# Optimization experiments

Measured on AMD Instinct MI355X. Metric: run time of the kernel, lower is better.

## Reference

```python
import jax, jax.numpy as jnp
import numpy as np

PADDING = 1
STRIDE = 1

def setup_inputs() -> dict:
    key = jax.random.key(0)
    k1, k2 = jax.random.split(key)
    x = jax.random.normal(k1, (32, 64, 64, 64), dtype=jnp.float32)
    # kaiming_normal fan_out, relu: std = sqrt(2 / (out_ch * k * k))
    fan_out = 128 * 3 * 3
    std = np.sqrt(2.0 / fan_out).astype(np.float32)
    weight = jax.random.normal(k2, (128, 64, 3, 3), dtype=jnp.float32) * std
    bias = jnp.zeros((128,), dtype=jnp.float32)
    return {"x": x, "weight": weight, "bias": bias}

def reference(x, weight, bias):
    # Faithful to the unfold+multiply+sum path, which computes a standard
    # cross-correlation conv2d (torch conv semantics) with stride/padding.
    out = jax.lax.conv_general_dilated(
        x, weight,
        window_strides=(STRIDE, STRIDE),
        padding=[(PADDING, PADDING), (PADDING, PADDING)],
        dimension_numbers=("NCHW", "OIHW", "NCHW"),
    )
    return out + bias[None, :, None, None]
```

## Files before the change

### kernel.cpp

```cpp
#include <hip/hip_runtime.h>


typedef short short8 __attribute__((ext_vector_type(8)));
typedef float f32x4  __attribute__((ext_vector_type(4)));

static __device__ __forceinline__ unsigned short f2bf(float f) {
    unsigned int u = __float_as_uint(f);
    u = (u + 0x7FFFu + ((u >> 16) & 1u)) >> 16;
    return (unsigned short)u;
}
static __device__ __forceinline__ unsigned int pk2(float lo, float hi) {
    return (unsigned int)f2bf(lo) | ((unsigned int)f2bf(hi) << 16);
}

__global__ __launch_bounds__(256)
void prep_x(const float* __restrict__ x, unsigned short* __restrict__ xT)
{
    __shared__ float T[64][65];
    const int h = blockIdx.x, n = blockIdx.y, tid = threadIdx.x;
    const size_t nbase = (size_t)n * 262144 + (size_t)h * 64;
    #pragma unroll
    for (int i = 0; i < 16; ++i) {
        int idx = tid + i * 256;
        int ci = idx >> 6, w = idx & 63;
        T[ci][w] = x[nbase + (size_t)ci * 4096 + w];
    }
    __syncthreads();
    const int w = tid >> 2, cg = tid & 3;
    unsigned int pk[8];
    #pragma unroll
    for (int k = 0; k < 8; ++k)
        pk[k] = pk2(T[cg * 16 + 2 * k][w], T[cg * 16 + 2 * k + 1][w]);
    unsigned short* dst = xT + (((size_t)n * 64 + h) * 64 + w) * 64 + cg * 16;
    uint4 a; a.x = pk[0]; a.y = pk[1]; a.z = pk[2]; a.w = pk[3];
    uint4 b; b.x = pk[4]; b.y = pk[5]; b.z = pk[6]; b.w = pk[7];
    *(uint4*)(dst)     = a;
    *(uint4*)(dst + 8) = b;
}

__global__ __launch_bounds__(256)
void prep_w(const float* __restrict__ w, unsigned short* __restrict__ wA)
{
    int t = blockIdx.x * 256 + threadIdx.x;
    if (t >= 73728) return;
    int j    = t & 7;
    int lane = (t >> 3) & 63;
    int mf   = (t >> 9) & 3;
    int c    = (t >> 11) & 1;
    int rest = t >> 12;
    int p    = rest % 9;
    int cb   = rest / 9;
    int co = cb * 64 + mf * 16 + (lane & 15);
    int ci = c * 32 + (lane >> 4) * 8 + j;
    wA[t] = f2bf(w[(size_t)(co * 64 + ci) * 9 + p]);
}

__global__ __launch_bounds__(512, 4)
void conv_mfma5(const unsigned short* __restrict__ xT,
                const unsigned short* __restrict__ wA,
                const float* __restrict__ bias,
                float* __restrict__ out)
{
    __shared__ __align__(16) char lds[50688];

    const int tid  = threadIdx.x;
    const int h0   = blockIdx.x * 4;
    const int n    = blockIdx.y;
    const int wid  = tid >> 6;
    const int cb   = wid >> 2;
    const int wrow = wid & 3;
    const int lane = tid & 63;
    const int l15  = lane & 15, l4 = lane >> 4;

    const unsigned short* xTn = xT + (size_t)n * 262144;
    const unsigned short* wAb = wA + (size_t)cb * 36864;

    {
        uint4 xreg[7];
        #pragma unroll
        for (int k = 0; k < 7; ++k) {
            int G = tid + k * 512;
            if (k < 6 || tid < 96) {
                int hp = G / 528, rem = G - hp * 528;
                int wp = rem >> 3, g = rem & 7;
                int gh = h0 + hp - 1, gw = wp - 1;
                uint4 v; v.x = v.y = v.z = v.w = 0u;
                if ((unsigned)gh < 64u && (unsigned)gw < 64u)
                    v = *(const uint4*)(xTn + ((gh * 64 + gw) * 64 + g * 8));
                xreg[k] = v;
            }
        }
        #pragma unroll
        for (int k = 0; k < 7; ++k) {
            int G = tid + k * 512;
            if (k < 6 || tid < 96) {
                int hp = G / 528, rem = G - hp * 528;
                int wp = rem >> 3, g = rem & 7;
                *(uint4*)(lds + (hp * 66 + wp) * 128 + ((g ^ (wp & 7)) * 16)) = xreg[k];
            }
        }
    }
    __syncthreads();

    f32x4 acc[4][4];
    #pragma unroll
    for (int mf = 0; mf < 4; ++mf)
        #pragma unroll
        for (int nf = 0; nf < 4; ++nf)
            acc[mf][nf] = (f32x4)0.0f;

    #pragma unroll
    for (int p = 0; p < 9; ++p) {
        const int kh = p / 3, kw = p - kh * 3;
        #pragma unroll
        for (int c = 0; c < 2; ++c) {
            short8 Af[4], Bf[4];
            #pragma unroll
            for (int mf = 0; mf < 4; ++mf)
                Af[mf] = *(const short8*)(wAb + ((((p * 2 + c) * 4 + mf) * 64 + lane) << 3));
            #pragma unroll
            for (int nf = 0; nf < 4; ++nf) {
                const int hp = wrow + kh;
                const int wp = nf * 16 + l15 + kw;
                Bf[nf] = *(const short8*)(lds + (hp * 66 + wp) * 128 + (((c * 4 + l4) ^ (wp & 7)) * 16));
            }
            __builtin_amdgcn_s_setprio(1);
            #pragma unroll
            for (int mf = 0; mf < 4; ++mf)
                #pragma unroll
                for (int nf = 0; nf < 4; ++nf)
                    acc[mf][nf] = __builtin_amdgcn_mfma_f32_16x16x32_bf16(
                        Af[mf], Bf[nf], acc[mf][nf], 0, 0, 0);
            __builtin_amdgcn_s_setprio(0);
        }
    }

    {
        const int h = h0 + wrow;
        #pragma unroll
        for (int mf = 0; mf < 4; ++mf) {
            const f32x4 bv4 = *(const f32x4*)(bias + cb * 64 + mf * 16 + l4 * 4);
            #pragma unroll
            for (int r = 0; r < 4; ++r) {
                const int co = cb * 64 + mf * 16 + l4 * 4 + r;
                float* orow = out + (((size_t)n * 128 + co) * 64 + h) * 64;
                const float bv = bv4[r];
                #pragma unroll
                for (int nf = 0; nf < 4; ++nf)
                    orow[nf * 16 + l15] = acc[mf][nf][r] + bv;
            }
        }
    }
}

__global__ __launch_bounds__(256, 4)
void conv2d_f32_tiled(const float* __restrict__ x,
                      const float* __restrict__ wgt,
                      const float* __restrict__ bias,
                      float* __restrict__ out)
{
    __shared__ float Xlds[8][10][66];
    __shared__ float Wlds[32][72];
    const int tid = threadIdx.x;
    const int co0 = blockIdx.x * 32, h0 = blockIdx.y * 8, n = blockIdx.z;
    const int tco = tid >> 6, lane = tid & 63;
    float acc[8][8];
    #pragma unroll
    for (int i = 0; i < 8; ++i)
        #pragma unroll
        for (int j = 0; j < 8; ++j) acc[i][j] = 0.0f;
    for (int cc = 0; cc < 8; ++cc) {
        const int ci0 = cc * 8;
        for (int idx = tid; idx < 8 * 10 * 66; idx += 256) {
            const int ww = idx % 66, t = idx / 66, hh = t % 10, ci = t / 10;
            const int gh = h0 + hh - 1, gw = ww - 1;
            float v = 0.0f;
            if ((unsigned)gh < 64u && (unsigned)gw < 64u)
                v = x[(((size_t)n * 64 + ci0 + ci) * 64 + gh) * 64 + gw];
            Xlds[ci][hh][ww] = v;
        }
        for (int idx = tid; idx < 32 * 72; idx += 256) {
            const int r = idx % 72, co = idx / 72;
            Wlds[co][r] = wgt[(size_t)(co0 + co) * 576 + ci0 * 9 + r];
        }
        __syncthreads();
        for (int ci = 0; ci < 8; ++ci)
            #pragma unroll
            for (int kh = 0; kh < 3; ++kh)
                #pragma unroll
                for (int kw = 0; kw < 3; ++kw) {
                    float wv[8];
                    #pragma unroll
                    for (int i = 0; i < 8; ++i) wv[i] = Wlds[tco * 8 + i][ci * 9 + kh * 3 + kw];
                    #pragma unroll
                    for (int j = 0; j < 8; ++j) {
                        const float xv = Xlds[ci][j + kh][lane + kw];
                        #pragma unroll
                        for (int i = 0; i < 8; ++i) acc[i][j] = fmaf(wv[i], xv, acc[i][j]);
                    }
                }
        __syncthreads();
    }
    #pragma unroll
    for (int i = 0; i < 8; ++i) {
        const int co = co0 + tco * 8 + i;
        const float b = bias[co];
        #pragma unroll
        for (int j = 0; j < 8; ++j)
            out[(((size_t)n * 128 + co) * 64 + (h0 + j)) * 64 + lane] = acc[i][j] + b;
    }
}

extern "C" void kernel_launch(void* const* d_in, const int* in_sizes, int n_in,
                              void* d_out, int out_size, void* d_ws, size_t ws_size,
                              hipStream_t stream)
{
    const float* x    = (const float*)d_in[0];
    const float* wgt  = (const float*)d_in[1];
    const float* bias = (const float*)d_in[2];
    float* out        = (float*)d_out;

    const size_t XT_BYTES = (size_t)32 * 64 * 64 * 64 * 2;
    const size_t WT_BYTES = (size_t)128 * 576 * 2;

    if (ws_size < XT_BYTES + WT_BYTES) {
        dim3 grid(4, 8, 32);
        conv2d_f32_tiled<<<grid, 256, 0, stream>>>(x, wgt, bias, out);
        return;
    }

    unsigned short* xT = (unsigned short*)d_ws;
    unsigned short* wA = (unsigned short*)((char*)d_ws + XT_BYTES);

    prep_x<<<dim3(64, 32), 256, 0, stream>>>(x, xT);
    prep_w<<<dim3((73728 + 255) / 256), 256, 0, stream>>>(wgt, wA);
    conv_mfma5<<<dim3(16, 32), 512, 0, stream>>>(xT, wA, bias, out);
}
```

Before: 42.71 us.

## Stage weights in LDS and double output rows per block in MFMA conv

The conv kernel now covers 8 output rows per block instead of 4, which doubles each wave's N tile to 8 fragments and halves the grid to 256 blocks. Weights are stored in a plain co-major bf16 layout. Each kernel-row phase stages them into swizzled LDS, and the next phase's weights are prefetched into registers while the current phase computes. The aim is to replace repeated global weight reads per MFMA step with LDS reads and to amortise the halo overhead. In exchange the kernel uses about 130KB of dynamic LDS and more accumulator registers, which lowers occupancy. There are also extra barriers, and 256 blocks may underfill the 256 CUs.

```diff
diff --git a/kernel.cpp b/kernel.cpp
--- a/kernel.cpp
+++ b/kernel.cpp
@@ -39,32 +39,30 @@
 }
 
 __global__ __launch_bounds__(256)
-void prep_w(const float* __restrict__ w, unsigned short* __restrict__ wA)
+void prep_w(const float* __restrict__ w, unsigned short* __restrict__ wT)
 {
     int t = blockIdx.x * 256 + threadIdx.x;
-    if (t >= 73728) return;
-    int j    = t & 7;
-    int lane = (t >> 3) & 63;
-    int mf   = (t >> 9) & 3;
-    int c    = (t >> 11) & 1;
-    int rest = t >> 12;
-    int p    = rest % 9;
-    int cb   = rest / 9;
-    int co = cb * 64 + mf * 16 + (lane & 15);
-    int ci = c * 32 + (lane >> 4) * 8 + j;
-    wA[t] = f2bf(w[(size_t)(co * 64 + ci) * 9 + p]);
-}
-
-__global__ __launch_bounds__(512, 4)
-void conv_mfma5(const unsigned short* __restrict__ xT,
-                const unsigned short* __restrict__ wA,
+    if (t >= 128 * 576) return;
+    int co = t / 576, r = t - co * 576;
+    int p = r >> 6, ci = r & 63;
+    wT[t] = f2bf(w[(size_t)(co * 64 + ci) * 9 + p]);
+}
+
+#define XBYTES 84480
+#define WBYTES 49152
+#define TOTAL_LDS (XBYTES + WBYTES)
+
+__global__ __launch_bounds__(512, 2)
+void conv_mfma7(const unsigned short* __restrict__ xT,
+                const unsigned short* __restrict__ wT,
                 const float* __restrict__ bias,
                 float* __restrict__ out)
 {
-    __shared__ __align__(16) char lds[50688];
+    extern __shared__ __align__(16) char lds[];
+    char* wl = lds + XBYTES;
 
     const int tid  = threadIdx.x;
-    const int h0   = blockIdx.x * 4;
+    const int h0   = blockIdx.x * 8;
     const int n    = blockIdx.y;
     const int wid  = tid >> 6;
     const int cb   = wid >> 2;
@@ -73,14 +71,29 @@
     const int l15  = lane & 15, l4 = lane >> 4;
 
     const unsigned short* xTn = xT + (size_t)n * 262144;
-    const unsigned short* wAb = wA + (size_t)cb * 36864;
 
     {
-        uint4 xreg[7];
-        #pragma unroll
-        for (int k = 0; k < 7; ++k) {
-            int G = tid + k * 512;
-            if (k < 6 || tid < 96) {
+        uint4 wreg[6];
+        #pragma unroll
+        for (int k = 0; k < 6; ++k) {
+            int G = tid + k * 512;
+            int g = G & 7, co = (G >> 3) & 127, pl = G >> 10;
+            wreg[k] = *(const uint4*)(wT + co * 576 + (pl * 64 + g * 8));
+        }
+        #pragma unroll
+        for (int k = 0; k < 6; ++k) {
+            int G = tid + k * 512;
+            int g = G & 7, co = (G >> 3) & 127, pl = G >> 10;
+            *(uint4*)(wl + (pl * 128 + co) * 128 + ((g ^ (co & 7)) * 16)) = wreg[k];
+        }
+    }
+
+    {
+        uint4 xreg[11];
+        #pragma unroll
+        for (int k = 0; k < 11; ++k) {
+            int G = tid + k * 512;
+            if (k < 10 || tid < 160) {
                 int hp = G / 528, rem = G - hp * 528;
                 int wp = rem >> 3, g = rem & 7;
                 int gh = h0 + hp - 1, gw = wp - 1;
@@ -91,9 +104,9 @@
             }
         }
         #pragma unroll
-        for (int k = 0; k < 7; ++k) {
-            int G = tid + k * 512;
-            if (k < 6 || tid < 96) {
+        for (int k = 0; k < 11; ++k) {
+            int G = tid + k * 512;
+            if (k < 10 || tid < 160) {
                 int hp = G / 528, rem = G - hp * 528;
                 int wp = rem >> 3, g = rem & 7;
                 *(uint4*)(lds + (hp * 66 + wp) * 128 + ((g ^ (wp & 7)) * 16)) = xreg[k];
@@ -102,52 +115,78 @@
     }
     __syncthreads();
 
-    f32x4 acc[4][4];
+    f32x4 acc[4][8];
     #pragma unroll
     for (int mf = 0; mf < 4; ++mf)
         #pragma unroll
-        for (int nf = 0; nf < 4; ++nf)
+        for (int nf = 0; nf < 8; ++nf)
             acc[mf][nf] = (f32x4)0.0f;
 
     #pragma unroll
-    for (int p = 0; p < 9; ++p) {
-        const int kh = p / 3, kw = p - kh * 3;
-        #pragma unroll
-        for (int c = 0; c < 2; ++c) {
-            short8 Af[4], Bf[4];
-            #pragma unroll
-            for (int mf = 0; mf < 4; ++mf)
-                Af[mf] = *(const short8*)(wAb + ((((p * 2 + c) * 4 + mf) * 64 + lane) << 3));
-            #pragma unroll
-            for (int nf = 0; nf < 4; ++nf) {
-                const int hp = wrow + kh;
-                const int wp = nf * 16 + l15 + kw;
-                Bf[nf] = *(const short8*)(lds + (hp * 66 + wp) * 128 + (((c * 4 + l4) ^ (wp & 7)) * 16));
-            }
-            __builtin_amdgcn_s_setprio(1);
-            #pragma unroll
-            for (int mf = 0; mf < 4; ++mf)
-                #pragma unroll
-                for (int nf = 0; nf < 4; ++nf)
-                    acc[mf][nf] = __builtin_amdgcn_mfma_f32_16x16x32_bf16(
-                        Af[mf], Bf[nf], acc[mf][nf], 0, 0, 0);
-            __builtin_amdgcn_s_setprio(0);
-        }
-    }
-
-    {
-        const int h = h0 + wrow;
-        #pragma unroll
-        for (int mf = 0; mf < 4; ++mf) {
-            const f32x4 bv4 = *(const f32x4*)(bias + cb * 64 + mf * 16 + l4 * 4);
-            #pragma unroll
-            for (int r = 0; r < 4; ++r) {
-                const int co = cb * 64 + mf * 16 + l4 * 4 + r;
-                float* orow = out + (((size_t)n * 128 + co) * 64 + h) * 64;
-                const float bv = bv4[r];
-                #pragma unroll
-                for (int nf = 0; nf < 4; ++nf)
-                    orow[nf * 16 + l15] = acc[mf][nf][r] + bv;
+    for (int ph = 0; ph < 3; ++ph) {
+        uint4 wreg[6];
+        if (ph < 2) {
+            #pragma unroll
+            for (int k = 0; k < 6; ++k) {
+                int G = tid + k * 512;
+                int g = G & 7, co = (G >> 3) & 127, pl = G >> 10;
+                wreg[k] = *(const uint4*)(wT + co * 576 + (((ph + 1) * 3 + pl) * 64 + g * 8));
+            }
+        }
+
+        #pragma unroll
+        for (int pl = 0; pl < 3; ++pl) {
+            #pragma unroll
+            for (int c = 0; c < 2; ++c) {
+                short8 Af[4], Bf[8];
+                #pragma unroll
+                for (int mf = 0; mf < 4; ++mf) {
+                    const int co = cb * 64 + mf * 16 + l15;
+                    Af[mf] = *(const short8*)(wl + (pl * 128 + co) * 128 +
+                                              (((c * 4 + l4) ^ (co & 7)) * 16));
+                }
+                #pragma unroll
+                for (int nf = 0; nf < 8; ++nf) {
+                    const int hp = wrow * 2 + (nf >> 2) + ph;
+                    const int wp = (nf & 3) * 16 + l15 + pl;
+                    Bf[nf] = *(const short8*)(lds + (hp * 66 + wp) * 128 +
+                                              (((c * 4 + l4) ^ (wp & 7)) * 16));
+                }
+                __builtin_amdgcn_s_setprio(1);
+                #pragma unroll
+                for (int mf = 0; mf < 4; ++mf)
+                    #pragma unroll
+                    for (int nf = 0; nf < 8; ++nf)
+                        acc[mf][nf] = __builtin_amdgcn_mfma_f32_16x16x32_bf16(
+                            Af[mf], Bf[nf], acc[mf][nf], 0, 0, 0);
+                __builtin_amdgcn_s_setprio(0);
+            }
+        }
+
+        if (ph < 2) {
+            __syncthreads();
+            #pragma unroll
+            for (int k = 0; k < 6; ++k) {
+                int G = tid + k * 512;
+                int g = G & 7, co = (G >> 3) & 127, pl = G >> 10;
+                *(uint4*)(wl + (pl * 128 + co) * 128 + ((g ^ (co & 7)) * 16)) = wreg[k];
+            }
+            __syncthreads();
+        }
+    }
+
+    #pragma unroll
+    for (int mf = 0; mf < 4; ++mf) {
+        const f32x4 bv4 = *(const f32x4*)(bias + cb * 64 + mf * 16 + l4 * 4);
+        #pragma unroll
+        for (int r = 0; r < 4; ++r) {
+            const int co = cb * 64 + mf * 16 + l4 * 4 + r;
+            const float bv = bv4[r];
+            #pragma unroll
+            for (int nf = 0; nf < 8; ++nf) {
+                const int h = h0 + wrow * 2 + (nf >> 2);
+                const int w = (nf & 3) * 16 + l15;
+                out[(((size_t)n * 128 + co) * 64 + h) * 64 + w] = acc[mf][nf][r] + bv;
             }
         }
     }
@@ -230,9 +269,12 @@
     }
 
     unsigned short* xT = (unsigned short*)d_ws;
-    unsigned short* wA = (unsigned short*)((char*)d_ws + XT_BYTES);
+    unsigned short* wT = (unsigned short*)((char*)d_ws + XT_BYTES);
+
+    (void)hipFuncSetAttribute((const void*)conv_mfma7,
+                              hipFuncAttributeMaxDynamicSharedMemorySize, TOTAL_LDS);
 
     prep_x<<<dim3(64, 32), 256, 0, stream>>>(x, xT);
-    prep_w<<<dim3((73728 + 255) / 256), 256, 0, stream>>>(wgt, wA);
-    conv_mfma5<<<dim3(16, 32), 512, 0, stream>>>(xT, wA, bias, out);
-}
+    prep_w<<<dim3((128 * 576 + 255) / 256), 256, 0, stream>>>(wgt, wT);
+    conv_mfma7<<<dim3(8, 32), 512, TOTAL_LDS, stream>>>(xT, wT, bias, out);
+}
```

Measured after the change: 52.45 us. 1.23x slower.

## Pre-pad and pre-swizzle input, double-buffer per-tap tiles via direct global-to-LDS loads

Applied to the files above, without the earlier changes.

The input is now pre-padded to 66x66 in a pre-swizzled bf16 layout, and the weights are written per tap in a swizzled row layout. This lets the conv kernel stream A and B tiles for each of the 9 filter taps straight into LDS with global_load_lds, double-buffered so the next tap's load overlaps the current tap's MFMAs. The conv kernel shrinks to 256 threads covering 2 output rows, launched as 1024 blocks with a block-index swizzle. In exchange it adds a __syncthreads per tap, re-fetches weights and input for every tap, and moves the bounds handling into the prep kernels.

```diff
diff --git a/kernel.cpp b/kernel.cpp
--- a/kernel.cpp
+++ b/kernel.cpp
@@ -12,12 +12,24 @@
 static __device__ __forceinline__ unsigned int pk2(float lo, float hi) {
     return (unsigned int)f2bf(lo) | ((unsigned int)f2bf(hi) << 16);
 }
+static __device__ __forceinline__ void gload16(const void* g, void* l) {
+    __builtin_amdgcn_global_load_lds(
+        (const __attribute__((address_space(1))) void*)g,
+        (__attribute__((address_space(3))) void*)l, 16, 0, 0);
+}
 
 __global__ __launch_bounds__(256)
-void prep_x(const float* __restrict__ x, unsigned short* __restrict__ xT)
-{
+void prep_xp(const float* __restrict__ x, unsigned short* __restrict__ xP)
+{
+    const int hp = blockIdx.x, n = blockIdx.y, tid = threadIdx.x;
+    unsigned short* rowBase = xP + (((size_t)n * 66 + hp) * 66) * 64;
+    if (hp == 0 || hp == 65) {
+        uint4 z; z.x = z.y = z.z = z.w = 0u;
+        for (int i = tid; i < 528; i += 256) ((uint4*)rowBase)[i] = z;
+        return;
+    }
     __shared__ float T[64][65];
-    const int h = blockIdx.x, n = blockIdx.y, tid = threadIdx.x;
+    const int h = hp - 1;
     const size_t nbase = (size_t)n * 262144 + (size_t)h * 64;
     #pragma unroll
     for (int i = 0; i < 16; ++i) {
@@ -26,80 +38,76 @@
         T[ci][w] = x[nbase + (size_t)ci * 4096 + w];
     }
     __syncthreads();
+    if (tid < 16) {
+        uint4 z; z.x = z.y = z.z = z.w = 0u;
+        int wp = (tid >> 3) * 65;
+        ((uint4*)(rowBase + wp * 64))[tid & 7] = z;
+    }
     const int w = tid >> 2, cg = tid & 3;
-    unsigned int pk[8];
-    #pragma unroll
-    for (int k = 0; k < 8; ++k)
-        pk[k] = pk2(T[cg * 16 + 2 * k][w], T[cg * 16 + 2 * k + 1][w]);
-    unsigned short* dst = xT + (((size_t)n * 64 + h) * 64 + w) * 64 + cg * 16;
-    uint4 a; a.x = pk[0]; a.y = pk[1]; a.z = pk[2]; a.w = pk[3];
-    uint4 b; b.x = pk[4]; b.y = pk[5]; b.z = pk[6]; b.w = pk[7];
-    *(uint4*)(dst)     = a;
-    *(uint4*)(dst + 8) = b;
+    const int wp = w + 1;
+    #pragma unroll
+    for (int t = 0; t < 2; ++t) {
+        const int g = cg * 2 + t;
+        uint4 v;
+        v.x = pk2(T[g*8+0][w], T[g*8+1][w]);
+        v.y = pk2(T[g*8+2][w], T[g*8+3][w]);
+        v.z = pk2(T[g*8+4][w], T[g*8+5][w]);
+        v.w = pk2(T[g*8+6][w], T[g*8+7][w]);
+        *(uint4*)(rowBase + wp * 64 + ((g ^ (wp & 7)) * 8)) = v;
+    }
 }
 
 __global__ __launch_bounds__(256)
-void prep_w(const float* __restrict__ w, unsigned short* __restrict__ wA)
+void prep_wS(const float* __restrict__ w, unsigned short* __restrict__ wS)
 {
     int t = blockIdx.x * 256 + threadIdx.x;
-    if (t >= 73728) return;
-    int j    = t & 7;
-    int lane = (t >> 3) & 63;
-    int mf   = (t >> 9) & 3;
-    int c    = (t >> 11) & 1;
-    int rest = t >> 12;
-    int p    = rest % 9;
-    int cb   = rest / 9;
-    int co = cb * 64 + mf * 16 + (lane & 15);
-    int ci = c * 32 + (lane >> 4) * 8 + j;
-    wA[t] = f2bf(w[(size_t)(co * 64 + ci) * 9 + p]);
-}
-
-__global__ __launch_bounds__(512, 4)
-void conv_mfma5(const unsigned short* __restrict__ xT,
-                const unsigned short* __restrict__ wA,
+    if (t >= 9216) return;
+    int gp = t & 7, p = (t >> 3) % 9, co = (t >> 3) / 9;
+    int g = gp ^ (co & 7);
+    uint4 v;
+    const float* src = w + (size_t)(co * 64 + g * 8) * 9 + p;
+    v.x = pk2(src[0*9], src[1*9]);
+    v.y = pk2(src[2*9], src[3*9]);
+    v.z = pk2(src[4*9], src[5*9]);
+    v.w = pk2(src[6*9], src[7*9]);
+    *(uint4*)(wS + (size_t)t * 8) = v;
+}
+
+#define ABYTES 16384
+#define BBYTES 16384
+#define BUFBYTES (ABYTES + BBYTES)
+#define TOTAL_LDS (2 * BUFBYTES)
+
+__global__ __launch_bounds__(256, 3)
+void conv_mfma8(const unsigned short* __restrict__ xP,
+                const unsigned short* __restrict__ wS,
                 const float* __restrict__ bias,
                 float* __restrict__ out)
 {
-    __shared__ __align__(16) char lds[50688];
+    extern __shared__ __align__(16) char lds[];
 
     const int tid  = threadIdx.x;
-    const int h0   = blockIdx.x * 4;
-    const int n    = blockIdx.y;
-    const int wid  = tid >> 6;
-    const int cb   = wid >> 2;
-    const int wrow = wid & 3;
-    const int lane = tid & 63;
+    const int bid  = blockIdx.x;
+    const int swz  = (bid & 7) * 128 + (bid >> 3);
+    const int n    = swz >> 5;
+    const int h0   = (swz & 31) * 2;
+    const int wid  = tid >> 6, lane = tid & 63;
+    const int cb   = wid >> 1;
+    const int sh   = wid & 1;
     const int l15  = lane & 15, l4 = lane >> 4;
 
-    const unsigned short* xTn = xT + (size_t)n * 262144;
-    const unsigned short* wAb = wA + (size_t)cb * 36864;
-
-    {
-        uint4 xreg[7];
-        #pragma unroll
-        for (int k = 0; k < 7; ++k) {
-            int G = tid + k * 512;
-            if (k < 6 || tid < 96) {
-                int hp = G / 528, rem = G - hp * 528;
-                int wp = rem >> 3, g = rem & 7;
-                int gh = h0 + hp - 1, gw = wp - 1;
-                uint4 v; v.x = v.y = v.z = v.w = 0u;
-                if ((unsigned)gh < 64u && (unsigned)gw < 64u)
-                    v = *(const uint4*)(xTn + ((gh * 64 + gw) * 64 + g * 8));
-                xreg[k] = v;
-            }
-        }
-        #pragma unroll
-        for (int k = 0; k < 7; ++k) {
-            int G = tid + k * 512;
-            if (k < 6 || tid < 96) {
-                int hp = G / 528, rem = G - hp * 528;
-                int wp = rem >> 3, g = rem & 7;
-                *(uint4*)(lds + (hp * 66 + wp) * 128 + ((g ^ (wp & 7)) * 16)) = xreg[k];
-            }
-        }
-    }
+    const char* aSrc = (const char*)wS +
+        ((size_t)(wid * 32 + (lane >> 3)) * 1152 + (lane & 7) * 16);
+    const char* bSrc = (const char*)xP +
+        ((((size_t)n * 66 + h0 + (wid >> 1)) * 66 + (wid & 1) * 32 + (lane >> 3)) * 128 +
+         (lane & 7) * 16);
+    char* aDst = lds + wid * 4096;
+    char* bDst = lds + ABYTES + wid * 4096;
+
+    #pragma unroll
+    for (int k = 0; k < 4; ++k) gload16(aSrc + k * 9216, aDst + k * 1024);
+    #pragma unroll
+    for (int k = 0; k < 4; ++k) gload16(bSrc + k * 1024, bDst + k * 1024);
     __syncthreads();
 
     f32x4 acc[4][4];
@@ -111,18 +119,32 @@
 
     #pragma unroll
     for (int p = 0; p < 9; ++p) {
-        const int kh = p / 3, kw = p - kh * 3;
+        const int kw = p % 3;
+        if (p < 8) {
+            const int pn  = p + 1;
+            const int off = ((pn / 3) * 66 + (pn % 3)) * 128;
+            char* aD = aDst + ((pn & 1) ? BUFBYTES : 0);
+            char* bD = bDst + ((pn & 1) ? BUFBYTES : 0);
+            #pragma unroll
+            for (int k = 0; k < 4; ++k) gload16(aSrc + pn * 128 + k * 9216, aD + k * 1024);
+            #pragma unroll
+            for (int k = 0; k < 4; ++k) gload16(bSrc + off + k * 1024, bD + k * 1024);
+        }
+
+        const char* A = lds + ((p & 1) ? BUFBYTES : 0);
+        const char* B = A + ABYTES;
         #pragma unroll
         for (int c = 0; c < 2; ++c) {
             short8 Af[4], Bf[4];
             #pragma unroll
-            for (int mf = 0; mf < 4; ++mf)
-                Af[mf] = *(const short8*)(wAb + ((((p * 2 + c) * 4 + mf) * 64 + lane) << 3));
+            for (int mf = 0; mf < 4; ++mf) {
+                const int co = cb * 64 + mf * 16 + l15;
+                Af[mf] = *(const short8*)(A + co * 128 + (((c * 4 + l4) ^ (co & 7)) * 16));
+            }
             #pragma unroll
             for (int nf = 0; nf < 4; ++nf) {
-                const int hp = wrow + kh;
-                const int wp = nf * 16 + l15 + kw;
-                Bf[nf] = *(const short8*)(lds + (hp * 66 + wp) * 128 + (((c * 4 + l4) ^ (wp & 7)) * 16));
+                const int sp = sh * 64 + nf * 16 + l15;
+                Bf[nf] = *(const short8*)(B + sp * 128 + (((c * 4 + l4) ^ ((sp + kw) & 7)) * 16));
             }
             __builtin_amdgcn_s_setprio(1);
             #pragma unroll
@@ -133,10 +155,11 @@
                         Af[mf], Bf[nf], acc[mf][nf], 0, 0, 0);
             __builtin_amdgcn_s_setprio(0);
         }
+        __syncthreads();
     }
 
     {
-        const int h = h0 + wrow;
+        const int h = h0 + sh;
         #pragma unroll
         for (int mf = 0; mf < 4; ++mf) {
             const f32x4 bv4 = *(const f32x4*)(bias + cb * 64 + mf * 16 + l4 * 4);
@@ -144,10 +167,9 @@
             for (int r = 0; r < 4; ++r) {
                 const int co = cb * 64 + mf * 16 + l4 * 4 + r;
                 float* orow = out + (((size_t)n * 128 + co) * 64 + h) * 64;
-                const float bv = bv4[r];
                 #pragma unroll
                 for (int nf = 0; nf < 4; ++nf)
-                    orow[nf * 16 + l15] = acc[mf][nf][r] + bv;
+                    orow[nf * 16 + l15] = acc[mf][nf][r] + bv4[r];
             }
         }
     }
@@ -220,19 +242,22 @@
     const float* bias = (const float*)d_in[2];
     float* out        = (float*)d_out;
 
-    const size_t XT_BYTES = (size_t)32 * 64 * 64 * 64 * 2;
-    const size_t WT_BYTES = (size_t)128 * 576 * 2;
-
-    if (ws_size < XT_BYTES + WT_BYTES) {
+    const size_t XP_BYTES = (size_t)32 * 66 * 66 * 64 * 2;
+    const size_t WS_BYTES = (size_t)128 * 9 * 64 * 2;
+
+    if (ws_size < XP_BYTES + WS_BYTES) {
         dim3 grid(4, 8, 32);
         conv2d_f32_tiled<<<grid, 256, 0, stream>>>(x, wgt, bias, out);
         return;
     }
 
-    unsigned short* xT = (unsigned short*)d_ws;
-    unsigned short* wA = (unsigned short*)((char*)d_ws + XT_BYTES);
-
-    prep_x<<<dim3(64, 32), 256, 0, stream>>>(x, xT);
-    prep_w<<<dim3((73728 + 255) / 256), 256, 0, stream>>>(wgt, wA);
-    conv_mfma5<<<dim3(16, 32), 512, 0, stream>>>(xT, wA, bias, out);
-}
+    unsigned short* xP = (unsigned short*)d_ws;
+    unsigned short* wS = (unsigned short*)((char*)d_ws + XP_BYTES);
+
+    (void)hipFuncSetAttribute((const void*)conv_mfma8,
+                              hipFuncAttributeMaxDynamicSharedMemorySize, TOTAL_LDS);
+
+    prep_xp<<<dim3(66, 32), 256, 0, stream>>>(x, xP);
+    prep_wS<<<dim3(36), 256, 0, stream>>>(wgt, wS);
+    conv_mfma8<<<dim3(1024), 256, TOTAL_LDS, stream>>>(xP, wS, bias, out);
+}
```

After: 44.15 us. 1.03x slower.
